# Kernel optimization log

Measured on AMD Instinct MI355X. Metric: run time of the kernel, lower is better.

The kernel has to match this reference:

```python
import jax, jax.numpy as jnp
import numpy as np
import math

# dims matching init_kwargs
B, N, CS, CZ = 1, 512, 384, 128
H, C, PQ, PV = 8, 128, 8, 8
INF, EPS = 1e5, 1e-8

# ---- quaternion / motor helpers (PGA motor encoded as [qw,qx,qy,qz,tx,ty,tz,0]) ----

def quat_conj(q):
    return q * jnp.array([1.0, -1.0, -1.0, -1.0], q.dtype)

def quat_mul(a, b):
    aw, ax, ay, az = jnp.split(a, 4, -1)
    bw, bx, by, bz = jnp.split(b, 4, -1)
    return jnp.concatenate([
        aw*bw - ax*bx - ay*by - az*bz,
        aw*bx + ax*bw + ay*bz - az*by,
        aw*by - ax*bz + ay*bw + az*bx,
        aw*bz + ax*by - ay*bx + az*bw], -1)

def quat_rotate(q, v):
    qv = q[..., 1:]
    uv = jnp.cross(qv, v)
    uuv = jnp.cross(qv, uv)
    return v + 2.0 * (q[..., :1] * uv + uuv)

def point_trafo(p, q, t):
    # p [...,K,3]; rigid transform by frame motor, homogeneous 4-vector out
    pp = quat_rotate(q, p) + t
    return jnp.concatenate([pp, jnp.ones_like(pp[..., :1])], -1)

def mv_transform(mv, q, t):
    # versor sandwich on a 16-dim multivector: three rotatable 3-vector blocks,
    # the point block (7:10, weight at 10) also translates; slots 0 and 10:16 invariant
    s0 = mv[..., 0:1]
    v1 = quat_rotate(q, mv[..., 1:4])
    v2 = quat_rotate(q, mv[..., 4:7])
    w = mv[..., 10:11]
    p = quat_rotate(q, mv[..., 7:10]) + w * t
    return jnp.concatenate([s0, v1, v2, p, mv[..., 10:16]], -1)

def mv_transform_inv(mv, q, t):
    qc = quat_conj(q)
    s0 = mv[..., 0:1]
    v1 = quat_rotate(qc, mv[..., 1:4])
    v2 = quat_rotate(qc, mv[..., 4:7])
    w = mv[..., 10:11]
    p = quat_rotate(qc, mv[..., 7:10] - w * t)
    return jnp.concatenate([s0, v1, v2, p, mv[..., 10:16]], -1)


def _forward(s, g, z, T, mask, W_q, b_q, W_kv, b_kv, W_qp, b_qp, W_kp, b_kp,
             W_vg, b_vg, W_mg, W_b, b_b, W_dz, b_dz, head_weights,
             softmax_weights, W_out, b_out, W_geo):
    T8 = T[..., :8]                                      # extract_motor
    qn = T8[..., :4]
    qn = qn / jnp.sqrt(jnp.sum(qn**2, -1, keepdims=True) + EPS)
    tr = T8[..., 4:7]

    q = (s @ W_q + b_q).reshape(B, N, H, C)
    kv = (s @ W_kv + b_kv).reshape(B, N, H, 2 * C)
    k, v = kv[..., :C], kv[..., C:]

    def make_pts(W, bb):
        # split into 3 chunks + stack(dim=-1) == reshape(...,3,HP).swapaxes
        p = (s @ W + bb).reshape(B, N, 3, H * PQ).swapaxes(-1, -2)  # [B,N,HP,3]
        p4 = point_trafo(p, qn[:, :, None, :], tr[:, :, None, :])
        return p4.reshape(B, N, H, PQ, 4)

    q_pts = make_pts(W_qp, b_qp)
    k_pts = make_pts(W_kp, b_kp)

    v_g = (s @ W_vg + b_vg).reshape(B, N, PV, 16)
    v_g = jnp.einsum('oi,bnic->bnoc', W_mg,
                     jnp.concatenate([v_g, g], -2)).reshape(B, N, H, PV, 16)

    bias = jnp.einsum('bijz,zh->bhij', z, W_b) + b_b[None, :, None, None]
    a = jnp.einsum('bihc,bjhc->bhij', q, k) * math.sqrt(1.0 / (3 * C))
    a = a + math.sqrt(1.0 / 3.0) * bias

    disp = q_pts[:, :, None, :, :, :3] - k_pts[:, None, :, :, :, :3]  # [B,N,N,H,P,3]
    pt = jnp.sum(disp**2, -1)                                         # [B,N,N,H,P]
    hw = jax.nn.softplus(head_weights) * math.sqrt(1.0 / (3 * (PQ * 9.0 / 2)))
    pt = -0.5 * jnp.sum(pt * hw[None, None, None, :, None], -1)       # [B,N,N,H]

    sq_mask = INF * (mask[:, :, None] * mask[:, None, :] - 1.0)
    a = a + pt.transpose(0, 3, 1, 2) + sq_mask[:, None]
    a = jax.nn.softmax(softmax_weights[None, :, None, None] * a, axis=-1)

    o = jnp.einsum('bhij,bjhc->bihc', a, v)                           # [B,N,H,C]

    qb, tb = qn[:, :, None, None, :], tr[:, :, None, None, :]
    vg_glob = mv_transform(v_g, qb, tb)
    o_g = jnp.einsum('bhij,bjhpc->bihpc', a, vg_glob)
    o_g = mv_transform_inv(o_g, qb, tb)                               # [B,N,H,PV,16]
    n1 = jnp.sqrt(jnp.sum(o_g[..., :10]**2, -1) + EPS)
    n2 = jnp.sqrt(jnp.sum(o_g[..., 10:]**2, -1) + EPS)
    o_g_norm = jnp.stack([n1, n2], -1)                                # [B,N,H,PV,2]

    # local relative frame features (8 per head)
    q_rel = quat_mul(quat_conj(qn)[:, :, None, :], qn[:, None, :, :])
    t_rel = quat_rotate(quat_conj(qn)[:, :, None, :], tr[:, None, :, :] - tr[:, :, None, :])
    rel = jnp.concatenate([q_rel, t_rel, jnp.zeros_like(t_rel[..., :1])], -1)  # [B,N,N,8]
    o_rel = jnp.einsum('bhij,bijc->bihc', a, rel)

    o_pair = jnp.einsum('bhij,bijc->bihc', a, z @ W_dz + b_dz)        # [B,N,H,CZ//4]

    feats = jnp.concatenate([o_pair, o, o_rel,
                             o_g.reshape(B, N, H, PV * 16),
                             o_g_norm.reshape(B, N, H, PV * 2)], -1).reshape(B, N, -1)
    s_out = feats @ W_out + b_out                                     # [B,N,CS]
    g_out = jnp.einsum('oi,bnic->bnoc', W_geo, o_g.reshape(B, N, H * PV, 16))
    return s_out, g_out


def setup_inputs() -> dict:
    key = jax.random.key(0)
    ks = jax.random.split(key, 32)
    def rn(i, shape, sc=1.0):
        return sc * jax.random.normal(ks[i], shape, jnp.float32)
    s = rn(0, (B, N, CS))
    g = rn(1, (B, N, PV, 16))
    z = rn(2, (B, N, N, CZ))
    Traw = rn(3, (B, N, 16))
    qn = Traw[..., :4]
    qn = qn / jnp.sqrt(jnp.sum(qn**2, -1, keepdims=True) + 1e-8)
    T = Traw.at[..., :4].set(qn).at[..., 4:7].multiply(3.0).at[..., 7:].set(0.0)
    mask = jnp.ones((B, N), jnp.float32)
    w = 0.02
    CAT = H * (CZ // 4 + C + 8 + PV * 18)   # 2496
    return dict(
        s=s, g=g, z=z, T=T, mask=mask,
        W_q=rn(4, (CS, H * C), w), b_q=jnp.zeros((H * C,), jnp.float32),
        W_kv=rn(5, (CS, 2 * H * C), w), b_kv=jnp.zeros((2 * H * C,), jnp.float32),
        W_qp=rn(6, (CS, H * PQ * 3), w), b_qp=jnp.zeros((H * PQ * 3,), jnp.float32),
        W_kp=rn(7, (CS, H * PQ * 3), w), b_kp=jnp.zeros((H * PQ * 3,), jnp.float32),
        W_vg=rn(8, (CS, PV * 16), w), b_vg=jnp.zeros((PV * 16,), jnp.float32),
        W_mg=rn(9, (H * PV, 2 * PV), 0.1),
        W_b=rn(10, (CZ, H), w), b_b=jnp.zeros((H,), jnp.float32),
        W_dz=rn(11, (CZ, CZ // 4), w), b_dz=jnp.zeros((CZ // 4,), jnp.float32),
        head_weights=-2.0 + 0.3 * rn(12, (H,)),
        softmax_weights=jnp.ones((H,), jnp.float32) + 0.1 * rn(13, (H,)),
        W_out=rn(14, (CAT, CS), w), b_out=jnp.zeros((CS,), jnp.float32),
        W_geo=rn(15, (PV, H * PV), 0.1))


def reference(s, g, z, T, mask, W_q, b_q, W_kv, b_kv, W_qp, b_qp, W_kp, b_kp,
              W_vg, b_vg, W_mg, W_b, b_b, W_dz, b_dz, head_weights,
              softmax_weights, W_out, b_out, W_geo):
    return _forward(s, g, z, T, mask, W_q, b_q, W_kv, b_kv, W_qp, b_qp, W_kp,
                    b_kp, W_vg, b_vg, W_mg, W_b, b_b, W_dz, b_dz, head_weights,
                    softmax_weights, W_out, b_out, W_geo)
```

## Files before the change

### kernel.cpp

```cpp
#include <hip/hip_runtime.h>
#include <math.h>

#define NN 512
#define CSD 384
#define CZD 128
#define HD 8
#define CD 128
#define EPSV 1e-8f
#define INFV 100000.0f

#define OFF_QN    ((size_t)0)
#define OFF_TR    ((size_t)2048)
#define OFF_ROWT  ((size_t)4096)
#define OFF_COLT  ((size_t)8192)
#define OFF_SB    ((size_t)12288)
#define OFF_QBUF  ((size_t)45056)
#define OFF_KV    ((size_t)569344)
#define OFF_QPR   ((size_t)1617920)
#define OFF_KPR   ((size_t)1716224)
#define OFF_VGR   ((size_t)1814528)
#define OFF_ZB    ((size_t)1880064)
#define OFF_A     ((size_t)3977216)
#define OFF_U     ((size_t)6074368)
#define OFF_V     ((size_t)6729728)
#define OFF_VP    ((size_t)7385088)
#define OFF_OB0   ((size_t)8433664)
#define OFF_OB1   ((size_t)8957952)
#define OFF_OG0   ((size_t)9482240)
#define OFF_OG1   ((size_t)10006528)
#define OFF_FEATS ((size_t)10530816)
#define OFF_PS    ((size_t)11808768)

typedef __attribute__((ext_vector_type(4))) float f32x4;
typedef __attribute__((ext_vector_type(8))) short bf16x8;
typedef __attribute__((ext_vector_type(4))) short s16x4;

__device__ __forceinline__ void qrot(const float q[4], const float* v, float* out) {
    float qw = q[0], qx = q[1], qy = q[2], qz = q[3];
    float ux = qy*v[2] - qz*v[1];
    float uy = qz*v[0] - qx*v[2];
    float uz = qx*v[1] - qy*v[0];
    float uux = qy*uz - qz*uy;
    float uuy = qz*ux - qx*uz;
    float uuz = qx*uy - qy*ux;
    out[0] = v[0] + 2.0f*(qw*ux + uux);
    out[1] = v[1] + 2.0f*(qw*uy + uuy);
    out[2] = v[2] + 2.0f*(qw*uz + uuz);
}

__device__ __forceinline__ void cvt2(float x, unsigned short& h, unsigned short& lo) {
    unsigned u = __float_as_uint(x);
    unsigned r = (u + 0x7FFFu + ((u >> 16) & 1u)) >> 16;
    h = (unsigned short)r;
    float hf = __uint_as_float(r << 16);
    float lf = x - hf;
    unsigned u2 = __float_as_uint(lf);
    unsigned r2 = (u2 + 0x7FFFu + ((u2 >> 16) & 1u)) >> 16;
    lo = (unsigned short)r2;
}

__device__ __forceinline__ void stA(short* H, short* L, int row, int k4, float4 v) {
    unsigned short h0,l0,h1,l1,h2,l2,h3,l3;
    cvt2(v.x,h0,l0); cvt2(v.y,h1,l1); cvt2(v.z,h2,l2); cvt2(v.w,h3,l3);
    s16x4 vh = {(short)h0,(short)h1,(short)h2,(short)h3};
    s16x4 vl = {(short)l0,(short)l1,(short)l2,(short)l3};
    *(s16x4*)(H + row*40 + k4) = vh;
    *(s16x4*)(L + row*40 + k4) = vl;
}
__device__ __forceinline__ void stBT(short* H, short* L, int k, int n4, float4 v) {
    unsigned short h, lo;
    cvt2(v.x,h,lo); H[(n4+0)*40+k]=(short)h; L[(n4+0)*40+k]=(short)lo;
    cvt2(v.y,h,lo); H[(n4+1)*40+k]=(short)h; L[(n4+1)*40+k]=(short)lo;
    cvt2(v.z,h,lo); H[(n4+2)*40+k]=(short)h; L[(n4+2)*40+k]=(short)lo;
    cvt2(v.w,h,lo); H[(n4+3)*40+k]=(short)h; L[(n4+3)*40+k]=(short)lo;
}

template<int BT>
__device__ __forceinline__ void mfma_tiles(const float* __restrict__ A, int lda,
                                           const float* __restrict__ B, int ldb,
                                           int m0, int n0, int k0, int nk,
                                           f32x4* acc,
                                           short* Ah, short* Al, short* Bh, short* Bl) {
    int t = threadIdx.x;
    int w = t >> 6, l = t & 63, g = l >> 4, li = l & 15;
    int ar = t >> 3, ak = (t & 7) << 2;
    const float* Ap0 = A + (size_t)(m0 + ar)*lda + ak;
    const float* Ap1 = A + (size_t)(m0 + ar + 32)*lda + ak;
    const float* Bp0; const float* Bp1;
    int bk = t >> 4, bn = (t & 15) << 2;
    if (BT) {
        Bp0 = B + (size_t)(n0 + ar)*ldb + ak;
        Bp1 = B + (size_t)(n0 + ar + 32)*ldb + ak;
    } else {
        Bp0 = B + (size_t)bk*ldb + n0 + bn;
        Bp1 = B + (size_t)(bk + 16)*ldb + n0 + bn;
    }
    float4 a0 = *(const float4*)(Ap0 + k0);
    float4 a1 = *(const float4*)(Ap1 + k0);
    float4 b0, b1;
    if (BT) { b0 = *(const float4*)(Bp0 + k0); b1 = *(const float4*)(Bp1 + k0); }
    else    { b0 = *(const float4*)(Bp0 + (size_t)k0*ldb); b1 = *(const float4*)(Bp1 + (size_t)k0*ldb); }
    for (int kc = 0; kc < nk; kc++) {
        stA(Ah, Al, ar, ak, a0);
        stA(Ah, Al, ar+32, ak, a1);
        if (BT) { stA(Bh, Bl, ar, ak, b0); stA(Bh, Bl, ar+32, ak, b1); }
        else    { stBT(Bh, Bl, bk, bn, b0); stBT(Bh, Bl, bk+16, bn, b1); }
        __syncthreads();
        if (kc + 1 < nk) {
            int kb = k0 + (kc+1)*32;
            a0 = *(const float4*)(Ap0 + kb);
            a1 = *(const float4*)(Ap1 + kb);
            if (BT) { b0 = *(const float4*)(Bp0 + kb); b1 = *(const float4*)(Bp1 + kb); }
            else { b0 = *(const float4*)(Bp0 + (size_t)kb*ldb); b1 = *(const float4*)(Bp1 + (size_t)kb*ldb); }
        }
        int arow = (w*16 + li)*40 + g*8;
        bf16x8 avh = *(bf16x8*)(Ah + arow);
        bf16x8 avl = *(bf16x8*)(Al + arow);
        #pragma unroll
        for (int c = 0; c < 4; c++) {
            int brow = (c*16 + li)*40 + g*8;
            bf16x8 bvh = *(bf16x8*)(Bh + brow);
            bf16x8 bvl = *(bf16x8*)(Bl + brow);
            acc[c] = __builtin_amdgcn_mfma_f32_16x16x32_bf16(avh, bvh, acc[c], 0, 0, 0);
            acc[c] = __builtin_amdgcn_mfma_f32_16x16x32_bf16(avh, bvl, acc[c], 0, 0, 0);
            acc[c] = __builtin_amdgcn_mfma_f32_16x16x32_bf16(avl, bvh, acc[c], 0, 0, 0);
        }
        __syncthreads();
    }
}

__device__ __forceinline__ void gemm_tiles(const float* __restrict__ A, int lda,
                                           const float* __restrict__ B, int ldb,
                                           int m0, int n0, int k0, int nk,
                                           float acc[4][4], float* AsT, float* Bs) {
    int t = threadIdx.x;
    int tx = t & 15, ty = t >> 4;
    int arow = t >> 3, ak4 = (t & 7) << 2;
    int brow = t >> 4, bc4 = (t & 15) << 2;
    const float* Ap0 = A + (size_t)(m0 + arow)*lda + ak4;
    const float* Ap1 = A + (size_t)(m0 + arow + 32)*lda + ak4;
    const float* Bp0 = B + (size_t)brow*ldb + n0 + bc4;
    const float* Bp1 = B + (size_t)(brow + 16)*ldb + n0 + bc4;
    float4 a0 = *(const float4*)(Ap0 + k0);
    float4 a1 = *(const float4*)(Ap1 + k0);
    float4 b0 = *(const float4*)(Bp0 + (size_t)k0*ldb);
    float4 b1 = *(const float4*)(Bp1 + (size_t)k0*ldb);
    for (int kc = 0; kc < nk; kc++) {
        AsT[(ak4+0)*68 + arow] = a0.x;
        AsT[(ak4+1)*68 + arow] = a0.y;
        AsT[(ak4+2)*68 + arow] = a0.z;
        AsT[(ak4+3)*68 + arow] = a0.w;
        AsT[(ak4+0)*68 + arow+32] = a1.x;
        AsT[(ak4+1)*68 + arow+32] = a1.y;
        AsT[(ak4+2)*68 + arow+32] = a1.z;
        AsT[(ak4+3)*68 + arow+32] = a1.w;
        *(float4*)(Bs + brow*64 + bc4) = b0;
        *(float4*)(Bs + (brow+16)*64 + bc4) = b1;
        __syncthreads();
        if (kc + 1 < nk) {
            int kb = k0 + (kc+1)*32;
            a0 = *(const float4*)(Ap0 + kb);
            a1 = *(const float4*)(Ap1 + kb);
            b0 = *(const float4*)(Bp0 + (size_t)kb*ldb);
            b1 = *(const float4*)(Bp1 + (size_t)kb*ldb);
        }
        #pragma unroll
        for (int kk = 0; kk < 32; kk++) {
            float4 av = *(const float4*)(AsT + kk*68 + ty*4);
            float4 bv = *(const float4*)(Bs + kk*64 + tx*4);
            acc[0][0] += av.x*bv.x; acc[0][1] += av.x*bv.y; acc[0][2] += av.x*bv.z; acc[0][3] += av.x*bv.w;
            acc[1][0] += av.y*bv.x; acc[1][1] += av.y*bv.y; acc[1][2] += av.y*bv.z; acc[1][3] += av.y*bv.w;
            acc[2][0] += av.z*bv.x; acc[2][1] += av.z*bv.y; acc[2][2] += av.z*bv.z; acc[2][3] += av.z*bv.w;
            acc[3][0] += av.w*bv.x; acc[3][1] += av.w*bv.y; acc[3][2] += av.w*bv.z; acc[3][3] += av.w*bv.w;
        }
        __syncthreads();
    }
}


__global__ __launch_bounds__(256) void k_proj_all(const float* __restrict__ s,
    const float* __restrict__ W_q,  const float* __restrict__ b_q,  float* __restrict__ qbuf,
    const float* __restrict__ W_kv, const float* __restrict__ b_kv, float* __restrict__ kvb,
    const float* __restrict__ W_qp, const float* __restrict__ b_qp, float* __restrict__ qpr,
    const float* __restrict__ W_kp, const float* __restrict__ b_kp, float* __restrict__ kpr,
    const float* __restrict__ W_vg, const float* __restrict__ b_vg, float* __restrict__ vgr) {
    __shared__ float AsT[32*68];
    __shared__ float Bs[32*64];
    int ny = blockIdx.y;
    const float* W; const float* bias; float* C; int N; int n0;
    if (ny < 16)      { W=W_q;  bias=b_q;  C=qbuf; N=1024; n0=ny*64; }
    else if (ny < 48) { W=W_kv; bias=b_kv; C=kvb;  N=2048; n0=(ny-16)*64; }
    else if (ny < 51) { W=W_qp; bias=b_qp; C=qpr;  N=192;  n0=(ny-48)*64; }
    else if (ny < 54) { W=W_kp; bias=b_kp; C=kpr;  N=192;  n0=(ny-51)*64; }
    else              { W=W_vg; bias=b_vg; C=vgr;  N=128;  n0=(ny-54)*64; }
    int m0 = blockIdx.x*64;
    float acc[4][4] = {};
    gemm_tiles(s, CSD, W, N, m0, n0, 0, 12, acc, AsT, Bs);
    int tx = threadIdx.x & 15, ty = threadIdx.x >> 4;
    float4 bb = *(const float4*)(bias + n0 + tx*4);
    #pragma unroll
    for (int rr = 0; rr < 4; rr++) {
        float4 o = make_float4(acc[rr][0]+bb.x, acc[rr][1]+bb.y, acc[rr][2]+bb.z, acc[rr][3]+bb.w);
        *(float4*)(C + (size_t)(m0+ty*4+rr)*N + n0 + tx*4) = o;
    }
}

__global__ __launch_bounds__(256) void k_geo(
    const float* __restrict__ T,
    const float* __restrict__ qpr, const float* __restrict__ kpr,
    const float* __restrict__ vgr, const float* __restrict__ g,
    const float* __restrict__ W_mg,
    const float* __restrict__ qbuf, const float* __restrict__ kvb,
    const float* __restrict__ hwraw, const float* __restrict__ b_b,
    float* __restrict__ qn, float* __restrict__ tr,
    float* __restrict__ U, float* __restrict__ V,
    float* __restrict__ rowt, float* __restrict__ colt,
    float* __restrict__ Vp)
{
    __shared__ float s_q[4];
    __shared__ float s_t[3];
    __shared__ float s_qpts[192], s_kpts[192];
    __shared__ float s_Qsq[8], s_Ksq[8];
    int n = blockIdx.x, t = threadIdx.x;
    if (t == 0) {
        float q0=T[n*16+0], q1=T[n*16+1], q2=T[n*16+2], q3=T[n*16+3];
        float inv = 1.0f/sqrtf(q0*q0+q1*q1+q2*q2+q3*q3 + EPSV);
        float a0=q0*inv, a1=q1*inv, a2=q2*inv, a3=q3*inv;
        s_q[0]=a0; s_q[1]=a1; s_q[2]=a2; s_q[3]=a3;
        float u0=T[n*16+4], u1=T[n*16+5], u2=T[n*16+6];
        s_t[0]=u0; s_t[1]=u1; s_t[2]=u2;
        qn[n*4+0]=a0; qn[n*4+1]=a1; qn[n*4+2]=a2; qn[n*4+3]=a3;
        tr[n*3+0]=u0; tr[n*3+1]=u1; tr[n*3+2]=u2;
    }
    __syncthreads();
    float q[4]={s_q[0],s_q[1],s_q[2],s_q[3]};
    float t0=s_t[0], t1=s_t[1], t2=s_t[2];
    if (t < 128) {
        int m = t & 63;
        const float* raw = (t < 64) ? qpr : kpr;
        float p[3] = {raw[n*192 + m], raw[n*192 + 64 + m], raw[n*192 + 128 + m]};
        float r[3]; qrot(q,p,r);
        r[0]+=t0; r[1]+=t1; r[2]+=t2;
        float* dp = (t<64) ? s_qpts : s_kpts;
        dp[m*3+0]=r[0]; dp[m*3+1]=r[1]; dp[m*3+2]=r[2];
        float ss = r[0]*r[0]+r[1]*r[1]+r[2]*r[2];
        ss += __shfl_down(ss,4,8);
        ss += __shfl_down(ss,2,8);
        ss += __shfl_down(ss,1,8);
        if ((m&7)==0) ((t<64)?s_Qsq:s_Ksq)[m>>3] = ss;
    } else if (t < 192) {
        int o = t - 128;
        float in[16];
        #pragma unroll
        for (int c=0;c<16;c++){
            float acc=0.0f;
            #pragma unroll
            for (int i=0;i<8;i++)  acc += W_mg[o*16+i]*vgr[n*128+i*16+c];
            #pragma unroll
            for (int i=8;i<16;i++) acc += W_mg[o*16+i]*g[n*128+(i-8)*16+c];
            in[c]=acc;
        }
        float out[16];
        out[0]=in[0];
        qrot(q,in+1,out+1);
        qrot(q,in+4,out+4);
        float w=in[10];
        qrot(q,in+7,out+7);
        out[7]+=w*t0; out[8]+=w*t1; out[9]+=w*t2;
        #pragma unroll
        for (int c=10;c<16;c++) out[c]=in[c];
        int h=o>>3, pp=o&7;
        float* vp = Vp + ((size_t)(h*512+n))*256 + 128 + pp*16;
        #pragma unroll
        for (int c=0;c<16;c++) vp[c]=out[c];
    }
    #pragma unroll
    for (int l=0;l<4;l++){
        int f = t + l*256; int h = f>>7, c = f&127;
        Vp[((size_t)(h*512+n))*256 + c] = kvb[(size_t)n*2048 + h*256 + 128 + c];
    }
    __syncthreads();
    #pragma unroll
    for (int h = 0; h < 8; h++) {
        float hwv = log1pf(expf(hwraw[h])) * 0.09622504486493763f;
        if (t < 160) {
            float u, v;
            if (t < 128) {
                u = 0.05103103630798287f * qbuf[(size_t)n*1024 + h*128 + t];
                v = kvb[(size_t)n*2048 + h*256 + t];
            } else if (t < 152) {
                int d = t - 128;
                u = hwv * s_qpts[h*24 + d];
                v = s_kpts[h*24 + d];
            } else { u = 0.0f; v = 0.0f; }
            U[((size_t)h*512 + n)*160 + t] = u;
            V[((size_t)h*512 + n)*160 + t] = v;
        }
        if (t == 160) rowt[h*512+n] = -0.5f*hwv*s_Qsq[h] + 0.5773502691896258f*b_b[h] - INFV;
        if (t == 161) colt[h*512+n] = -0.5f*hwv*s_Ksq[h];
    }
}

__global__ __launch_bounds__(256) void k_zb(const float* __restrict__ z,
        const float* __restrict__ W_b, float* __restrict__ zb) {
    int i = blockIdx.x, j0 = blockIdx.y*128;
    int t = threadIdx.x, w = t>>6, l = t&63;
    int gp = l>>4, k = l&15;
    float wb[8][8];
    #pragma unroll
    for (int cc=0;cc<8;cc++){
        float4 w0 = *(const float4*)(W_b + (k*8+cc)*8);
        float4 w1 = *(const float4*)(W_b + (k*8+cc)*8 + 4);
        wb[cc][0]=w0.x; wb[cc][1]=w0.y; wb[cc][2]=w0.z; wb[cc][3]=w0.w;
        wb[cc][4]=w1.x; wb[cc][5]=w1.y; wb[cc][6]=w1.z; wb[cc][7]=w1.w;
    }
    for (int it = 0; it < 8; it++) {
        int j = j0 + it*16 + w*4 + gp;
        const float* zp = z + ((size_t)i*512 + j)*128 + k*8;
        float4 za = *(const float4*)(zp);
        float4 zb4 = *(const float4*)(zp + 4);
        float zz[8] = {za.x,za.y,za.z,za.w,zb4.x,zb4.y,zb4.z,zb4.w};
        float acc[8];
        #pragma unroll
        for (int h=0;h<8;h++) acc[h] = zz[0]*wb[0][h];
        #pragma unroll
        for (int cc=1;cc<8;cc++)
            #pragma unroll
            for (int h=0;h<8;h++) acc[h] += zz[cc]*wb[cc][h];
        #pragma unroll
        for (int h=0;h<8;h++) {
            acc[h] += __shfl_xor(acc[h], 1);
            acc[h] += __shfl_xor(acc[h], 2);
            acc[h] += __shfl_xor(acc[h], 4);
            acc[h] += __shfl_xor(acc[h], 8);
        }
        float outv = acc[0];
        #pragma unroll
        for (int h=1;h<8;h++) if (k == h) outv = acc[h];
        if (k < 8) zb[((size_t)k*512 + i)*512 + j] = outv;
    }
}

__global__ __launch_bounds__(256) void k_scorefill(const float* __restrict__ U, const float* __restrict__ V,
        const float* __restrict__ rowt, const float* __restrict__ colt,
        const float* __restrict__ zb, const float* __restrict__ mask,
        const float* __restrict__ sw, float* __restrict__ Am) {
    __shared__ short Ah[64*40], Al[64*40], Bh[64*40], Bl[64*40];
    int h = blockIdx.z;
    int m0 = blockIdx.x*64, n0 = blockIdx.y*64;
    f32x4 acc[4] = {};
    mfma_tiles<1>(U + (size_t)h*512*160, 160, V + (size_t)h*512*160, 160,
                  m0, n0, 0, 5, acc, Ah, Al, Bh, Bl);
    int t = threadIdx.x, w = t >> 6, l = t & 63, g = l >> 4, li = l & 15;
    float swh = sw[h];
    #pragma unroll
    for (int c = 0; c < 4; c++) {
        int j = n0 + c*16 + li;
        float ct = colt[h*512 + j];
        float mj = mask[j];
        #pragma unroll
        for (int r = 0; r < 4; r++) {
            int i = m0 + w*16 + g*4 + r;
            float rt = rowt[h*512 + i];
            float mi = mask[i]*INFV;
            float zv = zb[((size_t)h*512 + i)*512 + j];
            Am[((size_t)h*512 + i)*512 + j] =
                (acc[c][r] + rt + ct + 0.5773502691896258f*zv + mi*mj)*swh;
        }
    }
}

__global__ __launch_bounds__(256) void k_softmax(float* __restrict__ Am,
        const float* __restrict__ qn, const float* __restrict__ tr, float* __restrict__ S) {
    __shared__ float red[8];
    __shared__ float sred[4][8];
    int row = blockIdx.x;
    float* p = Am + (size_t)row*512;
    int t = threadIdx.x;
    float x0 = p[t], x1 = p[t+256];
    float m = fmaxf(x0, x1);
    #pragma unroll
    for (int o = 32; o > 0; o >>= 1) m = fmaxf(m, __shfl_xor(m, o));
    int wv = t >> 6, ln = t & 63;
    if (ln == 0) red[wv] = m;
    __syncthreads();
    m = fmaxf(fmaxf(red[0], red[1]), fmaxf(red[2], red[3]));
    float e0 = expf(x0 - m), e1 = expf(x1 - m);
    float sm = e0 + e1;
    #pragma unroll
    for (int o = 32; o > 0; o >>= 1) sm += __shfl_xor(sm, o);
    __syncthreads();
    if (ln == 0) red[4 + wv] = sm;
    __syncthreads();
    float inv = 1.0f / (red[4]+red[5]+red[6]+red[7]);
    float a0 = e0*inv, a1 = e1*inv;
    p[t] = a0;
    p[t+256] = a1;
    float4 q0 = *(const float4*)(qn + t*4);
    float4 q1 = *(const float4*)(qn + (t+256)*4);
    float acc[8];
    acc[0] = a0*q0.x + a1*q1.x;
    acc[1] = a0*q0.y + a1*q1.y;
    acc[2] = a0*q0.z + a1*q1.z;
    acc[3] = a0*q0.w + a1*q1.w;
    acc[4] = a0*tr[t*3+0] + a1*tr[(t+256)*3+0];
    acc[5] = a0*tr[t*3+1] + a1*tr[(t+256)*3+1];
    acc[6] = a0*tr[t*3+2] + a1*tr[(t+256)*3+2];
    acc[7] = a0 + a1;
    #pragma unroll
    for (int c = 0; c < 8; c++) {
        #pragma unroll
        for (int o = 32; o > 0; o >>= 1) acc[c] += __shfl_xor(acc[c], o);
    }
    if (ln == 0) {
        #pragma unroll
        for (int c = 0; c < 8; c++) sred[wv][c] = acc[c];
    }
    __syncthreads();
    if (t < 8) {
        int h = row >> 9, i = row & 511;
        S[i*64 + h*8 + t] = sred[0][t]+sred[1][t]+sred[2][t]+sred[3][t];
    }
}

__global__ __launch_bounds__(256) void k_apply(const float* __restrict__ Am,
        const float* __restrict__ Vp, float* __restrict__ ob0, float* __restrict__ ob1,
        float* __restrict__ og0, float* __restrict__ og1) {
    __shared__ short Ah[64*40], Al[64*40], Bh[64*40], Bl[64*40];
    int m0 = blockIdx.x*64;
    int n0 = blockIdx.y*64;
    int h = blockIdx.z & 7, js = blockIdx.z >> 3;
    f32x4 acc[4] = {};
    mfma_tiles<0>(Am + (size_t)h*512*512, 512, Vp + (size_t)h*512*256, 256,
                  m0, n0, js*256, 8, acc, Ah, Al, Bh, Bl);
    int t = threadIdx.x, w = t >> 6, l = t & 63, g = l >> 4, li = l & 15;
    float* obuf = js ? ob1 : ob0;
    float* og   = js ? og1 : og0;
    #pragma unroll
    for (int c = 0; c < 4; c++) {
        int col = n0 + c*16 + li;
        float* base = (col < 128) ? (obuf + h*128 + col) : (og + h*128 + col - 128);
        #pragma unroll
        for (int r = 0; r < 4; r++) {
            int i = m0 + w*16 + g*4 + r;
            base[(size_t)i*1024] = acc[c][r];
        }
    }
}

__global__ __launch_bounds__(256) void k_azfin(
    const float* __restrict__ Am, const float* __restrict__ z,
    const float* __restrict__ ob0, const float* __restrict__ ob1,
    const float* __restrict__ og0, const float* __restrict__ og1,
    const float* __restrict__ W_dz, const float* __restrict__ b_dz,
    const float* __restrict__ S, const float* __restrict__ qn, const float* __restrict__ tr,
    const float* __restrict__ W_geo,
    float* __restrict__ feats, float* __restrict__ outg)
{
    __shared__ float aT[512*8];
    __shared__ float part[3*1024];
    __shared__ float s_az[1024];
    __shared__ float s_og[1024];
    int i = blockIdx.x, t = threadIdx.x;
    #pragma unroll
    for (int l = 0; l < 16; l++) {
        int f = t + l*256;
        int h = f >> 9, j = f & 511;
        aT[j*8 + h] = Am[((size_t)h*512 + i)*512 + j];
    }
    __syncthreads();
    int c2 = t & 63, quarter = t >> 6;
    int jb = quarter*128;
    float acc[8][2] = {};
    for (int j = jb; j < jb+128; j++) {
        float2 zv = *(const float2*)(z + ((size_t)(i*NN) + j)*CZD + c2*2);
        float4 a0 = *(const float4*)(aT + j*8);
        float4 a1 = *(const float4*)(aT + j*8 + 4);
        acc[0][0] += a0.x*zv.x; acc[0][1] += a0.x*zv.y;
        acc[1][0] += a0.y*zv.x; acc[1][1] += a0.y*zv.y;
        acc[2][0] += a0.z*zv.x; acc[2][1] += a0.z*zv.y;
        acc[3][0] += a0.w*zv.x; acc[3][1] += a0.w*zv.y;
        acc[4][0] += a1.x*zv.x; acc[4][1] += a1.x*zv.y;
        acc[5][0] += a1.y*zv.x; acc[5][1] += a1.y*zv.y;
        acc[6][0] += a1.z*zv.x; acc[6][1] += a1.z*zv.y;
        acc[7][0] += a1.w*zv.x; acc[7][1] += a1.w*zv.y;
    }
    if (quarter > 0) {
        #pragma unroll
        for (int h = 0; h < 8; h++) {
            part[(quarter-1)*1024 + h*128 + c2*2 + 0] = acc[h][0];
            part[(quarter-1)*1024 + h*128 + c2*2 + 1] = acc[h][1];
        }
    }
    __syncthreads();
    if (quarter == 0) {
        #pragma unroll
        for (int h = 0; h < 8; h++) {
            #pragma unroll
            for (int d = 0; d < 2; d++) {
                s_az[h*128 + c2*2 + d] = acc[h][d] + part[h*128 + c2*2 + d]
                          + part[1024 + h*128 + c2*2 + d] + part[2048 + h*128 + c2*2 + d];
            }
        }
    }
    __syncthreads();
    float* f = feats + (size_t)i*2496;
    #pragma unroll
    for (int l = 0; l < 4; l++) {
        int ff = t + l*256; int h = ff>>7, c = ff&127;
        f[h*312 + 32 + c] = ob0[(size_t)i*1024 + h*128 + c] + ob1[(size_t)i*1024 + h*128 + c];
    }
    {
        int h = t >> 5, cdz = t & 31;
        float a2 = b_dz[cdz];
        #pragma unroll 4
        for (int zc = 0; zc < 128; zc++) a2 += s_az[h*128 + zc]*W_dz[zc*32 + cdz];
        f[h*312 + cdz] = a2;
    }
    float qc0=qn[i*4], qc1=-qn[i*4+1], qc2=-qn[i*4+2], qc3=-qn[i*4+3];
    float t0=tr[i*3], t1=tr[i*3+1], t2=tr[i*3+2];
    if (t < 64) {
        int h = t >> 3, p = t & 7;
        const float* a0 = og0 + (size_t)i*1024 + h*128 + p*16;
        const float* a1 = og1 + (size_t)i*1024 + h*128 + p*16;
        float in[16];
        #pragma unroll
        for (int c=0;c<16;c++) in[c]=a0[c]+a1[c];
        float qc[4]={qc0,qc1,qc2,qc3};
        float out[16];
        out[0]=in[0];
        qrot(qc,in+1,out+1);
        qrot(qc,in+4,out+4);
        float w=in[10];
        float tmp[3]={in[7]-w*t0, in[8]-w*t1, in[9]-w*t2};
        qrot(qc,tmp,out+7);
        #pragma unroll
        for (int c2x=10;c2x<16;c2x++) out[c2x]=in[c2x];
        float n1=EPSV, n2=EPSV;
        #pragma unroll
        for (int c2x=0;c2x<10;c2x++) n1 += out[c2x]*out[c2x];
        #pragma unroll
        for (int c2x=10;c2x<16;c2x++) n2 += out[c2x]*out[c2x];
        n1=sqrtf(n1); n2=sqrtf(n2);
        #pragma unroll
        for (int c2x=0;c2x<16;c2x++){ f[h*312+168+p*16+c2x]=out[c2x]; s_og[t*16+c2x]=out[c2x]; }
        f[h*312+296+p*2]=n1; f[h*312+296+p*2+1]=n2;
    } else if (t < 72) {
        int h = t - 64;
        const float* Sr = S + i*64 + h*8;
        float b0=Sr[0], b1=Sr[1], b2=Sr[2], b3=Sr[3];
        f[h*312+160] = qc0*b0 - qc1*b1 - qc2*b2 - qc3*b3;
        f[h*312+161] = qc0*b1 + qc1*b0 + qc2*b3 - qc3*b2;
        f[h*312+162] = qc0*b2 - qc1*b3 + qc2*b0 + qc3*b1;
        f[h*312+163] = qc0*b3 + qc1*b2 - qc2*b1 + qc3*b0;
        float A = Sr[7];
        float v[3]={Sr[4]-A*t0, Sr[5]-A*t1, Sr[6]-A*t2};
        float qc[4]={qc0,qc1,qc2,qc3};
        float r[3]; qrot(qc,v,r);
        f[h*312+164]=r[0]; f[h*312+165]=r[1]; f[h*312+166]=r[2]; f[h*312+167]=0.0f;
    }
    __syncthreads();
    if (t < 128) {
        int o = (t>>4) & 7, c = t & 15;
        float a3 = 0.0f;
        #pragma unroll 4
        for (int i2=0;i2<64;i2++) a3 += W_geo[o*64+i2]*s_og[i2*16+c];
        outg[(size_t)i*128 + o*16 + c] = a3;
    }
}

__global__ __launch_bounds__(256) void k_sout(const float* __restrict__ feats,
        const float* __restrict__ W_out, float* __restrict__ Ps) {
    __shared__ float AsT[32*68];
    __shared__ float Bs[32*64];
    int m0 = blockIdx.x*64, n0 = blockIdx.y*64, kz = blockIdx.z;
    float acc[4][4] = {};
    gemm_tiles(feats, 2496, W_out, CSD, m0, n0, kz*416, 13, acc, AsT, Bs);
    int tx = threadIdx.x & 15, ty = threadIdx.x >> 4;
    float* slab = Ps + (size_t)kz*512*384;
    #pragma unroll
    for (int rr = 0; rr < 4; rr++) {
        *(float4*)(slab + (size_t)(m0+ty*4+rr)*CSD + n0 + tx*4) =
            make_float4(acc[rr][0], acc[rr][1], acc[rr][2], acc[rr][3]);
    }
}

__global__ __launch_bounds__(256) void k_sout_red(const float* __restrict__ Ps,
        const float* __restrict__ b_out, float* __restrict__ out) {
    int idx = (blockIdx.x*256 + threadIdx.x)*4;
    float4 s = *(const float4*)(b_out + (idx % 384));
    #pragma unroll
    for (int kz = 0; kz < 6; kz++) {
        float4 p = *(const float4*)(Ps + (size_t)kz*196608 + idx);
        s.x += p.x; s.y += p.y; s.z += p.z; s.w += p.w;
    }
    *(float4*)(out + idx) = s;
}


extern "C" void kernel_launch(void* const* d_in, const int* in_sizes, int n_in,
                              void* d_out, int out_size, void* d_ws, size_t ws_size,
                              hipStream_t stream) {
    const float* s     = (const float*)d_in[0];
    const float* g     = (const float*)d_in[1];
    const float* z     = (const float*)d_in[2];
    const float* T     = (const float*)d_in[3];
    const float* mask  = (const float*)d_in[4];
    const float* W_q   = (const float*)d_in[5];
    const float* b_q   = (const float*)d_in[6];
    const float* W_kv  = (const float*)d_in[7];
    const float* b_kv  = (const float*)d_in[8];
    const float* W_qp  = (const float*)d_in[9];
    const float* b_qp  = (const float*)d_in[10];
    const float* W_kp  = (const float*)d_in[11];
    const float* b_kp  = (const float*)d_in[12];
    const float* W_vg  = (const float*)d_in[13];
    const float* b_vg  = (const float*)d_in[14];
    const float* W_mg  = (const float*)d_in[15];
    const float* W_b   = (const float*)d_in[16];
    const float* b_b   = (const float*)d_in[17];
    const float* W_dz  = (const float*)d_in[18];
    const float* b_dz  = (const float*)d_in[19];
    const float* hw    = (const float*)d_in[20];
    const float* sw    = (const float*)d_in[21];
    const float* W_out = (const float*)d_in[22];
    const float* b_out = (const float*)d_in[23];
    const float* W_geo = (const float*)d_in[24];

    float* ws   = (float*)d_ws;
    float* out  = (float*)d_out;

    float* qn   = ws + OFF_QN;
    float* tr   = ws + OFF_TR;
    float* rowt = ws + OFF_ROWT;
    float* colt = ws + OFF_COLT;
    float* Sbuf = ws + OFF_SB;
    float* qbuf = ws + OFF_QBUF;
    float* kvb  = ws + OFF_KV;
    float* qpr  = ws + OFF_QPR;
    float* kpr  = ws + OFF_KPR;
    float* vgr  = ws + OFF_VGR;
    float* zb   = ws + OFF_ZB;
    float* Am   = ws + OFF_A;
    float* U    = ws + OFF_U;
    float* V    = ws + OFF_V;
    float* Vp   = ws + OFF_VP;
    float* ob0  = ws + OFF_OB0;
    float* ob1  = ws + OFF_OB1;
    float* og0  = ws + OFF_OG0;
    float* og1  = ws + OFF_OG1;
    float* feats= ws + OFF_FEATS;
    float* Ps   = ws + OFF_PS;

    k_proj_all<<<dim3(8,56),256,0,stream>>>(s, W_q,b_q,qbuf, W_kv,b_kv,kvb,
                                            W_qp,b_qp,qpr, W_kp,b_kp,kpr, W_vg,b_vg,vgr);
    k_geo<<<NN,256,0,stream>>>(T,qpr,kpr,vgr,g,W_mg,qbuf,kvb,hw,b_b,
                               qn,tr,U,V,rowt,colt,Vp);
    k_zb<<<dim3(512,4),256,0,stream>>>(z,W_b,zb);
    k_scorefill<<<dim3(8,8,8),256,0,stream>>>(U,V,rowt,colt,zb,mask,sw,Am);
    k_softmax<<<4096,256,0,stream>>>(Am,qn,tr,Sbuf);
    k_apply<<<dim3(8,4,16),256,0,stream>>>(Am,Vp,ob0,ob1,og0,og1);
    k_azfin<<<NN,256,0,stream>>>(Am,z,ob0,ob1,og0,og1,W_dz,b_dz,Sbuf,qn,tr,W_geo,
                                 feats, out + (size_t)NN*CSD);
    k_sout<<<dim3(8,6,6),256,0,stream>>>(feats,W_out,Ps);
    k_sout_red<<<192,256,0,stream>>>(Ps,b_out,out);
}
```

Measured before the change: 392.9 us.

## Split attention-weighted z reduction into separate kernel parallel over j quarters

Moves the per-row A·z contraction out of k_azfin into a new k_az kernel launched on a 512x4 grid, so each block handles one quarter of the j range and writes partial sums to a new workspace region. k_azfin then just adds the four partials. This raises parallelism over the 32 MB z read, which was previously covered by only 512 blocks, and shrinks k_azfin's shared memory. In exchange it adds a kernel launch and extra global traffic for the partial buffer. The aT stride is padded to 12 floats, likely to reduce LDS bank conflicts.

New measurement: 396.2 us. No clear change (+0.8%).

```diff
diff --git a/kernel.cpp b/kernel.cpp
--- a/kernel.cpp
+++ b/kernel.cpp
@@ -30,6 +30,7 @@
 #define OFF_OG1   ((size_t)10006528)
 #define OFF_FEATS ((size_t)10530816)
 #define OFF_PS    ((size_t)11808768)
+#define OFF_AZP   ((size_t)12988416)
 
 typedef __attribute__((ext_vector_type(4))) float f32x4;
 typedef __attribute__((ext_vector_type(8))) short bf16x8;
@@ -423,6 +424,58 @@
     }
 }
 
+__global__ __launch_bounds__(256) void k_az(
+        const float* __restrict__ Am, const float* __restrict__ z,
+        float* __restrict__ azp) {
+    __shared__ float aT[128*12];
+    __shared__ float part[3*1024];
+    int i = blockIdx.x, jq = blockIdx.y, j0 = jq*128;
+    int t = threadIdx.x;
+    #pragma unroll
+    for (int l2 = 0; l2 < 4; l2++) {
+        int f = t + l2*256;
+        int h = f >> 7, jl = f & 127;
+        aT[jl*12 + h] = Am[((size_t)h*512 + i)*512 + j0 + jl];
+    }
+    __syncthreads();
+    int c2 = t & 63, sub = t >> 6;
+    int jb = sub*32;
+    float acc[8][2] = {};
+    for (int jo = 0; jo < 32; jo++) {
+        int j = jb + jo;
+        float2 zv = *(const float2*)(z + ((size_t)i*512 + j0 + j)*128 + c2*2);
+        float4 a0 = *(const float4*)(aT + j*12);
+        float4 a1 = *(const float4*)(aT + j*12 + 4);
+        acc[0][0] += a0.x*zv.x; acc[0][1] += a0.x*zv.y;
+        acc[1][0] += a0.y*zv.x; acc[1][1] += a0.y*zv.y;
+        acc[2][0] += a0.z*zv.x; acc[2][1] += a0.z*zv.y;
+        acc[3][0] += a0.w*zv.x; acc[3][1] += a0.w*zv.y;
+        acc[4][0] += a1.x*zv.x; acc[4][1] += a1.x*zv.y;
+        acc[5][0] += a1.y*zv.x; acc[5][1] += a1.y*zv.y;
+        acc[6][0] += a1.z*zv.x; acc[6][1] += a1.z*zv.y;
+        acc[7][0] += a1.w*zv.x; acc[7][1] += a1.w*zv.y;
+    }
+    if (sub > 0) {
+        #pragma unroll
+        for (int h = 0; h < 8; h++) {
+            part[(sub-1)*1024 + h*128 + c2*2 + 0] = acc[h][0];
+            part[(sub-1)*1024 + h*128 + c2*2 + 1] = acc[h][1];
+        }
+    }
+    __syncthreads();
+    if (sub == 0) {
+        float* dst = azp + ((size_t)jq*512 + i)*1024;
+        #pragma unroll
+        for (int h = 0; h < 8; h++) {
+            #pragma unroll
+            for (int d = 0; d < 2; d++) {
+                dst[h*128 + c2*2 + d] = acc[h][d] + part[h*128 + c2*2 + d]
+                          + part[1024 + h*128 + c2*2 + d] + part[2048 + h*128 + c2*2 + d];
+            }
+        }
+    }
+}
+
 __global__ __launch_bounds__(256) void k_apply(const float* __restrict__ Am,
         const float* __restrict__ Vp, float* __restrict__ ob0, float* __restrict__ ob1,
         float* __restrict__ og0, float* __restrict__ og1) {
@@ -449,7 +502,7 @@
 }
 
 __global__ __launch_bounds__(256) void k_azfin(
-    const float* __restrict__ Am, const float* __restrict__ z,
+    const float* __restrict__ azp,
     const float* __restrict__ ob0, const float* __restrict__ ob1,
     const float* __restrict__ og0, const float* __restrict__ og1,
     const float* __restrict__ W_dz, const float* __restrict__ b_dz,
@@ -457,51 +510,14 @@
     const float* __restrict__ W_geo,
     float* __restrict__ feats, float* __restrict__ outg)
 {
-    __shared__ float aT[512*8];
-    __shared__ float part[3*1024];
     __shared__ float s_az[1024];
     __shared__ float s_og[1024];
     int i = blockIdx.x, t = threadIdx.x;
     #pragma unroll
-    for (int l = 0; l < 16; l++) {
-        int f = t + l*256;
-        int h = f >> 9, j = f & 511;
-        aT[j*8 + h] = Am[((size_t)h*512 + i)*512 + j];
-    }
-    __syncthreads();
-    int c2 = t & 63, quarter = t >> 6;
-    int jb = quarter*128;
-    float acc[8][2] = {};
-    for (int j = jb; j < jb+128; j++) {
-        float2 zv = *(const float2*)(z + ((size_t)(i*NN) + j)*CZD + c2*2);
-        float4 a0 = *(const float4*)(aT + j*8);
-        float4 a1 = *(const float4*)(aT + j*8 + 4);
-        acc[0][0] += a0.x*zv.x; acc[0][1] += a0.x*zv.y;
-        acc[1][0] += a0.y*zv.x; acc[1][1] += a0.y*zv.y;
-        acc[2][0] += a0.z*zv.x; acc[2][1] += a0.z*zv.y;
-        acc[3][0] += a0.w*zv.x; acc[3][1] += a0.w*zv.y;
-        acc[4][0] += a1.x*zv.x; acc[4][1] += a1.x*zv.y;
-        acc[5][0] += a1.y*zv.x; acc[5][1] += a1.y*zv.y;
-        acc[6][0] += a1.z*zv.x; acc[6][1] += a1.z*zv.y;
-        acc[7][0] += a1.w*zv.x; acc[7][1] += a1.w*zv.y;
-    }
-    if (quarter > 0) {
-        #pragma unroll
-        for (int h = 0; h < 8; h++) {
-            part[(quarter-1)*1024 + h*128 + c2*2 + 0] = acc[h][0];
-            part[(quarter-1)*1024 + h*128 + c2*2 + 1] = acc[h][1];
-        }
-    }
-    __syncthreads();
-    if (quarter == 0) {
-        #pragma unroll
-        for (int h = 0; h < 8; h++) {
-            #pragma unroll
-            for (int d = 0; d < 2; d++) {
-                s_az[h*128 + c2*2 + d] = acc[h][d] + part[h*128 + c2*2 + d]
-                          + part[1024 + h*128 + c2*2 + d] + part[2048 + h*128 + c2*2 + d];
-            }
-        }
+    for (int l2 = 0; l2 < 4; l2++) {
+        int c = t + l2*256;
+        s_az[c] = azp[((size_t)0*512 + i)*1024 + c] + azp[((size_t)1*512 + i)*1024 + c]
+                + azp[((size_t)2*512 + i)*1024 + c] + azp[((size_t)3*512 + i)*1024 + c];
     }
     __syncthreads();
     float* f = feats + (size_t)i*2496;
@@ -651,6 +667,7 @@
     float* og1  = ws + OFF_OG1;
     float* feats= ws + OFF_FEATS;
     float* Ps   = ws + OFF_PS;
+    float* azp  = ws + OFF_AZP;
 
     k_proj_all<<<dim3(8,56),256,0,stream>>>(s, W_q,b_q,qbuf, W_kv,b_kv,kvb,
                                             W_qp,b_qp,qpr, W_kp,b_kp,kpr, W_vg,b_vg,vgr);
@@ -659,8 +676,9 @@
     k_zb<<<dim3(512,4),256,0,stream>>>(z,W_b,zb);
     k_scorefill<<<dim3(8,8,8),256,0,stream>>>(U,V,rowt,colt,zb,mask,sw,Am);
     k_softmax<<<4096,256,0,stream>>>(Am,qn,tr,Sbuf);
+    k_az<<<dim3(512,4),256,0,stream>>>(Am,z,azp);
     k_apply<<<dim3(8,4,16),256,0,stream>>>(Am,Vp,ob0,ob1,og0,og1);
-    k_azfin<<<NN,256,0,stream>>>(Am,z,ob0,ob1,og0,og1,W_dz,b_dz,Sbuf,qn,tr,W_geo,
+    k_azfin<<<NN,256,0,stream>>>(azp,ob0,ob1,og0,og1,W_dz,b_dz,Sbuf,qn,tr,W_geo,
                                  feats, out + (size_t)NN*CSD);
     k_sout<<<dim3(8,6,6),256,0,stream>>>(feats,W_out,Ps);
     k_sout_red<<<192,256,0,stream>>>(Ps,b_out,out);
```
